# Kernel tuning notes

Measured on AMD Instinct MI355X. Metric: run time of the kernel, lower is better.

## Reference

```python
import jax, jax.numpy as jnp
import numpy as np

B, R, A, S, F, N = 2, 1, 16, 14, 1024, 512  # batch, num_rx, num_rx_ant, ofdm_symbols, fft_size, num_effective_sc
D = S * N  # flattened time-frequency dim that C acts on


def setup_inputs() -> dict:
    key = jax.random.key(0)
    k0, k1, k2, k3 = jax.random.split(key, 4)
    scale = 1.0 / np.sqrt(D).astype(np.float32)
    x_re = jax.random.normal(k0, (B, R, A, S, F), jnp.float32)
    x_im = jax.random.normal(k1, (B, R, A, S, F), jnp.float32)
    C_re = jax.random.normal(k2, (D, D), jnp.float32) * scale
    C_im = jax.random.normal(k3, (D, D), jnp.float32) * scale
    # unique, sorted effective-subcarrier indices (as in an OFDM ResourceGrid)
    sc_ind = jnp.asarray(np.sort(np.random.default_rng(0).choice(F, N, replace=False)), jnp.int32)
    return {"x_re": x_re, "x_im": x_im, "C_re": C_re, "C_im": C_im, "sc_ind": sc_ind}


def reference(x_re, x_im, C_re, C_im, sc_ind):
    x = jax.lax.complex(x_re, x_im)            # [B,R,A,S,F] complex64
    C = jax.lax.complex(C_re, C_im)            # [D,D]
    y = jnp.take(x, sc_ind, axis=-1)           # gather effective subcarriers -> [B,R,A,S,N]
    b, r, a, s, n = y.shape
    yf = y.reshape(b, r, a, s * n)             # flatten_last_dims(y, 2)
    # multiply_from_right with adjoint: yf @ C^H
    yf = jnp.einsum('brad,ed->brae', yf, jnp.conj(C))
    y = yf.reshape(b, r, a, s, n)
    # scatter back into full fft_size grid (unique indices -> set == scatter_nd on zeros)
    out = jnp.zeros((b, r, a, s, F), y.dtype).at[..., sc_ind].set(y)
    return jnp.stack([out.real, out.imag])     # [2,B,R,A,S,F] (real, imag)
```

## Files before the change

### kernel.cpp

```cpp
#include <hip/hip_runtime.h>
#include <hip/hip_bf16.h>

#define B_ 2
#define R_ 1
#define A_ 16
#define S_ 14
#define F_ 1024
#define N_ 512
#define D_ (S_*N_)
#define M_ (B_*R_*A_)
#define KK_ (2*D_)
#define BE 64
#define ETILES (D_/BE)

typedef __attribute__((ext_vector_type(8))) short bf16x8;
typedef __attribute__((ext_vector_type(4))) float f32x4;

static __device__ inline short f2bf(float f) {
    __hip_bfloat16 h = __float2bfloat16(f);
    return *reinterpret_cast<short*>(&h);
}
static __device__ inline float bf2f(short s) {
    unsigned int u = ((unsigned int)(unsigned short)s) << 16;
    return __uint_as_float(u);
}

#define LDSP(p) ((__attribute__((address_space(3))) void*)(p))
#define GLBP(p) ((const __attribute__((address_space(1))) void*)(p))

__global__ void prep_kernel(const float* __restrict__ xr, const float* __restrict__ xi,
                            const int* __restrict__ sc, short* __restrict__ Ap) {
    int idx = blockIdx.x * blockDim.x + threadIdx.x;
    if (idx >= 64 * KK_) return;
    int k = idx % KK_;
    int r = idx / KK_;
    int m = r & 31;
    int half = (k >= D_) ? 1 : 0;
    int d = half ? (k - D_) : k;
    int s = d >> 9;
    int n = d & 511;
    int f = sc[n];
    const float* base = (r < 32) ? (half ? xi : xr) : (half ? xr : xi);
    float v = base[(m * S_ + s) * F_ + f];
    if (r >= 32 && half) v = -v;
    Ap[((size_t)(k >> 3) * 64 + r) * 8 + (k & 7)] = f2bf(v);
}

__global__ void zero_kernel(float4* __restrict__ out, int n4) {
    int i = blockIdx.x * blockDim.x + threadIdx.x;
    if (i < n4) out[i] = make_float4(0.f, 0.f, 0.f, 0.f);
}

__global__ __launch_bounds__(256) void gemm_wasync(
    const short* __restrict__ Ap,
    const float* __restrict__ Cre, const float* __restrict__ Cim,
    short* __restrict__ part_all)
{
    constexpr int KSPLIT = 28;
    constexpr int KBLK = KK_ / KSPLIT;
    constexpr int NCH  = KBLK / 32;
    __shared__ float Bl[4][3][16 * 32];
    __shared__ short Al[4][3][64 * 32];

    const int etile = blockIdx.x;
    const int ks    = blockIdx.y;
    const int tid   = threadIdx.x;
    const int wave  = tid >> 6;
    const int lane  = tid & 63;
    const int l16   = lane & 15;
    const int kg    = lane >> 4;

    const float* Cp = (ks < 14) ? Cre : Cim;
    const int kc = (ks % 14) * KBLK;
    const int ka = ks * KBLK;

    const int U0 = lane, U1 = 64 + lane;
    const float* bsrc0 = Cp + (size_t)(etile * 64 + wave * 16 + (U0 >> 3)) * D_
                            + kc + ((U0 & 7) ^ ((U0 >> 3) & 7)) * 4;
    const float* bsrc1 = Cp + (size_t)(etile * 64 + wave * 16 + (U1 >> 3)) * D_
                            + kc + ((U1 & 7) ^ ((U1 >> 3) & 7)) * 4;
    const short* asrc = Ap + (size_t)(ka >> 3) * 512 + lane * 8;

#define WAITV(n) asm volatile("s_waitcnt vmcnt(" #n ")" ::: "memory")
#define STAGE(cc) do { \
        int bb = (cc) % 3; \
        __builtin_amdgcn_global_load_lds(GLBP(bsrc0 + (size_t)(cc) * 32), \
                                         LDSP(&Bl[wave][bb][lane * 4]), 16, 0, 0); \
        __builtin_amdgcn_global_load_lds(GLBP(bsrc1 + (size_t)(cc) * 32), \
                                         LDSP(&Bl[wave][bb][(64 + lane) * 4]), 16, 0, 0); \
        __builtin_amdgcn_global_load_lds(GLBP(asrc + (size_t)(cc) * 2048 + 0 * 512), \
                                         LDSP(&Al[wave][bb][lane * 8]), 16, 0, 0); \
        __builtin_amdgcn_global_load_lds(GLBP(asrc + (size_t)(cc) * 2048 + 1 * 512), \
                                         LDSP(&Al[wave][bb][(64 + lane) * 8]), 16, 0, 0); \
        __builtin_amdgcn_global_load_lds(GLBP(asrc + (size_t)(cc) * 2048 + 2 * 512), \
                                         LDSP(&Al[wave][bb][(128 + lane) * 8]), 16, 0, 0); \
        __builtin_amdgcn_global_load_lds(GLBP(asrc + (size_t)(cc) * 2048 + 3 * 512), \
                                         LDSP(&Al[wave][bb][(192 + lane) * 8]), 16, 0, 0); \
    } while (0)

    STAGE(0);
    STAGE(1);
    STAGE(2);

    f32x4 acc0 = {0.f,0.f,0.f,0.f}, acc1 = {0.f,0.f,0.f,0.f};
    f32x4 acc2 = {0.f,0.f,0.f,0.f}, acc3 = {0.f,0.f,0.f,0.f};

    const int swz  = l16 & 7;
    const int boff = l16 * 32;
    const int u0x = ((kg * 2 + 0) ^ swz) * 4;
    const int u1x = ((kg * 2 + 1) ^ swz) * 4;

    for (int c = 0; c < NCH; ++c) {
        if (c <= NCH - 3)      { WAITV(12); }
        else if (c == NCH - 2) { WAITV(6); }
        else                   { WAITV(0); }
        __builtin_amdgcn_sched_barrier(0);

        const int buf = c % 3;
        f32x4 b0 = *reinterpret_cast<const f32x4*>(&Bl[wave][buf][boff + u0x]);
        f32x4 b1 = *reinterpret_cast<const f32x4*>(&Bl[wave][buf][boff + u1x]);
        bf16x8 a0 = *reinterpret_cast<const bf16x8*>(&Al[wave][buf][(kg * 64 + 0 * 16 + l16) * 8]);
        bf16x8 a1 = *reinterpret_cast<const bf16x8*>(&Al[wave][buf][(kg * 64 + 1 * 16 + l16) * 8]);
        bf16x8 a2 = *reinterpret_cast<const bf16x8*>(&Al[wave][buf][(kg * 64 + 2 * 16 + l16) * 8]);
        bf16x8 a3 = *reinterpret_cast<const bf16x8*>(&Al[wave][buf][(kg * 64 + 3 * 16 + l16) * 8]);
        asm volatile("s_waitcnt lgkmcnt(0)" ::: "memory");
        __builtin_amdgcn_sched_barrier(0);

        if (c + 3 < NCH) STAGE(c + 3);
        __builtin_amdgcn_sched_barrier(0);

        bf16x8 bfv;
        bfv[0] = f2bf(b0.x); bfv[1] = f2bf(b0.y); bfv[2] = f2bf(b0.z); bfv[3] = f2bf(b0.w);
        bfv[4] = f2bf(b1.x); bfv[5] = f2bf(b1.y); bfv[6] = f2bf(b1.z); bfv[7] = f2bf(b1.w);
        acc0 = __builtin_amdgcn_mfma_f32_16x16x32_bf16(a0, bfv, acc0, 0, 0, 0);
        acc1 = __builtin_amdgcn_mfma_f32_16x16x32_bf16(a1, bfv, acc1, 0, 0, 0);
        acc2 = __builtin_amdgcn_mfma_f32_16x16x32_bf16(a2, bfv, acc2, 0, 0, 0);
        acc3 = __builtin_amdgcn_mfma_f32_16x16x32_bf16(a3, bfv, acc3, 0, 0, 0);
    }
#undef STAGE
#undef WAITV

    const int e_lane = etile * 64 + wave * 16 + l16;
    short* part = part_all + (size_t)ks * (64 * D_);
    #pragma unroll
    for (int mt = 0; mt < 4; ++mt) {
        f32x4 a = (mt == 0) ? acc0 : (mt == 1) ? acc1 : (mt == 2) ? acc2 : acc3;
        int rbase = mt * 16 + kg * 4;
        #pragma unroll
        for (int r = 0; r < 4; ++r)
            part[(size_t)(rbase + r) * D_ + e_lane] = f2bf(a[r]);
    }
}

template<int KSPLIT, int PARTIALS>
__global__ __launch_bounds__(256) void gemm_sync(
    const short* __restrict__ Ap,
    const float* __restrict__ Cre, const float* __restrict__ Cim,
    const int* __restrict__ sc,
    void* __restrict__ outp)
{
    constexpr int KBLK = KK_ / KSPLIT;
    constexpr int NCH  = KBLK / 32;
    __shared__ float Bls[3][64 * 32];
    __shared__ short Als[3][64 * 32];

    const int etile = blockIdx.x;
    const int ks    = blockIdx.y;
    const int tid   = threadIdx.x;
    const int wave  = tid >> 6;
    const int lane  = tid & 63;
    const int l16   = lane & 15;
    const int kg    = lane >> 4;

    const float* Cp = (ks < KSPLIT / 2) ? Cre : Cim;
    const int kc = (ks % (KSPLIT / 2)) * KBLK;
    const int ka = ks * KBLK;

    const float* bsrc[2];
    #pragma unroll
    for (int q = 0; q < 2; ++q) {
        int U = q * 256 + tid;
        int row = U >> 3;
        int u = (U & 7) ^ (row & 7);
        bsrc[q] = Cp + (size_t)(etile * BE + row) * D_ + kc + u * 4;
    }
    const short* asrc = Ap + ((size_t)(ka >> 3) * 64) * 8 + tid * 8;

#define STG(c) do { \
        int bf_ = (c) % 3; \
        __builtin_amdgcn_global_load_lds(GLBP(bsrc[0] + (size_t)(c) * 32), \
                                         LDSP(&Bls[bf_][(0 * 256 + tid) * 4]), 16, 0, 0); \
        __builtin_amdgcn_global_load_lds(GLBP(bsrc[1] + (size_t)(c) * 32), \
                                         LDSP(&Bls[bf_][(1 * 256 + tid) * 4]), 16, 0, 0); \
        __builtin_amdgcn_global_load_lds(GLBP(asrc + (size_t)(c) * 2048), \
                                         LDSP(&Als[bf_][tid * 8]), 16, 0, 0); \
    } while (0)

    STG(0);
    STG(1);

    f32x4 acc0 = {0.f,0.f,0.f,0.f}, acc1 = {0.f,0.f,0.f,0.f};
    f32x4 acc2 = {0.f,0.f,0.f,0.f}, acc3 = {0.f,0.f,0.f,0.f};

    const int row  = wave * 16 + l16;
    const int swz  = row & 7;
    const int boff = row * 32;
    const int u0 = ((kg * 2 + 0) ^ swz) * 4;
    const int u1 = ((kg * 2 + 1) ^ swz) * 4;

    for (int c = 0; c < NCH; ++c) {
        if (c < NCH - 1) asm volatile("s_waitcnt vmcnt(3)" ::: "memory");
        else             asm volatile("s_waitcnt vmcnt(0)" ::: "memory");
        __builtin_amdgcn_sched_barrier(0);
        __builtin_amdgcn_s_barrier();

        const int buf = c % 3;
        f32x4 b0 = *reinterpret_cast<const f32x4*>(&Bls[buf][boff + u0]);
        f32x4 b1 = *reinterpret_cast<const f32x4*>(&Bls[buf][boff + u1]);
        bf16x8 a0 = *reinterpret_cast<const bf16x8*>(&Als[buf][(kg * 64 + 0 * 16 + l16) * 8]);
        bf16x8 a1 = *reinterpret_cast<const bf16x8*>(&Als[buf][(kg * 64 + 1 * 16 + l16) * 8]);
        bf16x8 a2 = *reinterpret_cast<const bf16x8*>(&Als[buf][(kg * 64 + 2 * 16 + l16) * 8]);
        bf16x8 a3 = *reinterpret_cast<const bf16x8*>(&Als[buf][(kg * 64 + 3 * 16 + l16) * 8]);
        asm volatile("s_waitcnt lgkmcnt(0)" ::: "memory");
        __builtin_amdgcn_sched_barrier(0);
        __builtin_amdgcn_s_barrier();

        if (c + 2 < NCH) STG(c + 2);

        bf16x8 bfv;
        bfv[0] = f2bf(b0.x); bfv[1] = f2bf(b0.y); bfv[2] = f2bf(b0.z); bfv[3] = f2bf(b0.w);
        bfv[4] = f2bf(b1.x); bfv[5] = f2bf(b1.y); bfv[6] = f2bf(b1.z); bfv[7] = f2bf(b1.w);
        acc0 = __builtin_amdgcn_mfma_f32_16x16x32_bf16(a0, bfv, acc0, 0, 0, 0);
        acc1 = __builtin_amdgcn_mfma_f32_16x16x32_bf16(a1, bfv, acc1, 0, 0, 0);
        acc2 = __builtin_amdgcn_mfma_f32_16x16x32_bf16(a2, bfv, acc2, 0, 0, 0);
        acc3 = __builtin_amdgcn_mfma_f32_16x16x32_bf16(a3, bfv, acc3, 0, 0, 0);
    }
#undef STG

    const int e_lane = etile * BE + row;
    if (PARTIALS) {
        short* part = (short*)outp + (size_t)ks * (64 * D_);
        #pragma unroll
        for (int mt = 0; mt < 4; ++mt) {
            f32x4 a = (mt == 0) ? acc0 : (mt == 1) ? acc1 : (mt == 2) ? acc2 : acc3;
            int rbase = mt * 16 + kg * 4;
            #pragma unroll
            for (int r = 0; r < 4; ++r)
                part[(size_t)(rbase + r) * D_ + e_lane] = f2bf(a[r]);
        }
    } else {
        float* out = (float*)outp;
        int s = e_lane >> 9, n = e_lane & 511;
        int f = sc[n];
        #pragma unroll
        for (int mt = 0; mt < 4; ++mt) {
            f32x4 a = (mt == 0) ? acc0 : (mt == 1) ? acc1 : (mt == 2) ? acc2 : acc3;
            int rbase = mt * 16 + kg * 4;
            #pragma unroll
            for (int r = 0; r < 4; ++r) {
                int rr = rbase + r;
                int pp = rr >> 5, m = rr & 31;
                atomicAdd(&out[((pp * M_ + m) * S_ + s) * F_ + f], a[r]);
            }
        }
    }
}

template<int KSPLIT>
__global__ void reduce_kernel(const short* __restrict__ part, const int* __restrict__ sc,
                              float* __restrict__ out) {
    int t = blockIdx.x * blockDim.x + threadIdx.x;
    if (t >= 64 * D_ / 8) return;
    int base = t * 8;
    int e0 = base % D_;
    int r  = base / D_;
    float v[8] = {0.f,0.f,0.f,0.f,0.f,0.f,0.f,0.f};
    #pragma unroll
    for (int ksp = 0; ksp < KSPLIT; ++ksp) {
        bf16x8 x = *reinterpret_cast<const bf16x8*>(&part[(size_t)ksp * (64 * D_) + base]);
        #pragma unroll
        for (int j = 0; j < 8; ++j) v[j] += bf2f(x[j]);
    }
    int pp = r >> 5, m = r & 31, s = e0 >> 9, n0 = e0 & 511;
    float* ob = &out[((pp * M_ + m) * S_ + s) * F_];
    #pragma unroll
    for (int j = 0; j < 8; ++j) ob[sc[n0 + j]] = v[j];
}

extern "C" void kernel_launch(void* const* d_in, const int* in_sizes, int n_in,
                              void* d_out, int out_size, void* d_ws, size_t ws_size,
                              hipStream_t stream) {
    const float* xr  = (const float*)d_in[0];
    const float* xi  = (const float*)d_in[1];
    const float* Cre = (const float*)d_in[2];
    const float* Cim = (const float*)d_in[3];
    const int*   sc  = (const int*)d_in[4];
    float* out = (float*)d_out;

    short* Ap = (short*)d_ws;
    const size_t partOff = 2u * 1024u * 1024u;
    const size_t need28  = partOff + 28ull * 64 * D_ * 2;
    const size_t need16  = partOff + 16ull * 64 * D_ * 2;

    prep_kernel<<<dim3((64 * KK_ + 255) / 256), 256, 0, stream>>>(xr, xi, sc, Ap);
    zero_kernel<<<dim3((917504 / 4 + 255) / 256), 256, 0, stream>>>((float4*)out, 917504 / 4);

    const int rthreads = 64 * D_ / 8;
    if (ws_size >= need28) {
        short* part = (short*)((char*)d_ws + partOff);
        gemm_wasync<<<dim3(ETILES, 28), 256, 0, stream>>>(Ap, Cre, Cim, part);
        reduce_kernel<28><<<dim3((rthreads + 255) / 256), 256, 0, stream>>>(part, sc, out);
    } else if (ws_size >= need16) {
        short* part = (short*)((char*)d_ws + partOff);
        gemm_sync<16, 1><<<dim3(ETILES, 16), 256, 0, stream>>>(Ap, Cre, Cim, sc, part);
        reduce_kernel<16><<<dim3((rthreads + 255) / 256), 256, 0, stream>>>(part, sc, out);
    } else {
        gemm_sync<16, 0><<<dim3(ETILES, 16), 256, 0, stream>>>(Ap, Cre, Cim, sc, out);
    }
}
```

Baseline: 123.8 us.

## Load GEMM A operand directly into registers instead of staging through LDS

Result: faster. 118.9 us (-4.0%).

```diff
diff --git a/kernel.cpp b/kernel.cpp
--- a/kernel.cpp
+++ b/kernel.cpp
@@ -51,7 +51,7 @@
     if (i < n4) out[i] = make_float4(0.f, 0.f, 0.f, 0.f);
 }
 
-__global__ __launch_bounds__(256) void gemm_wasync(
+__global__ __launch_bounds__(256, 2) void gemm_areg(
     const short* __restrict__ Ap,
     const float* __restrict__ Cre, const float* __restrict__ Cim,
     short* __restrict__ part_all)
@@ -60,7 +60,6 @@
     constexpr int KBLK = KK_ / KSPLIT;
     constexpr int NCH  = KBLK / 32;
     __shared__ float Bl[4][3][16 * 32];
-    __shared__ short Al[4][3][64 * 32];
 
     const int etile = blockIdx.x;
     const int ks    = blockIdx.y;
@@ -79,7 +78,7 @@
                             + kc + ((U0 & 7) ^ ((U0 >> 3) & 7)) * 4;
     const float* bsrc1 = Cp + (size_t)(etile * 64 + wave * 16 + (U1 >> 3)) * D_
                             + kc + ((U1 & 7) ^ ((U1 >> 3) & 7)) * 4;
-    const short* asrc = Ap + (size_t)(ka >> 3) * 512 + lane * 8;
+    const short* abase = Ap + (((size_t)(ka >> 3) + kg) * 64 + l16) * 8;
 
 #define WAITV(n) asm volatile("s_waitcnt vmcnt(" #n ")" ::: "memory")
 #define STAGE(cc) do { \
@@ -88,19 +87,7 @@
                                          LDSP(&Bl[wave][bb][lane * 4]), 16, 0, 0); \
         __builtin_amdgcn_global_load_lds(GLBP(bsrc1 + (size_t)(cc) * 32), \
                                          LDSP(&Bl[wave][bb][(64 + lane) * 4]), 16, 0, 0); \
-        __builtin_amdgcn_global_load_lds(GLBP(asrc + (size_t)(cc) * 2048 + 0 * 512), \
-                                         LDSP(&Al[wave][bb][lane * 8]), 16, 0, 0); \
-        __builtin_amdgcn_global_load_lds(GLBP(asrc + (size_t)(cc) * 2048 + 1 * 512), \
-                                         LDSP(&Al[wave][bb][(64 + lane) * 8]), 16, 0, 0); \
-        __builtin_amdgcn_global_load_lds(GLBP(asrc + (size_t)(cc) * 2048 + 2 * 512), \
-                                         LDSP(&Al[wave][bb][(128 + lane) * 8]), 16, 0, 0); \
-        __builtin_amdgcn_global_load_lds(GLBP(asrc + (size_t)(cc) * 2048 + 3 * 512), \
-                                         LDSP(&Al[wave][bb][(192 + lane) * 8]), 16, 0, 0); \
     } while (0)
-
-    STAGE(0);
-    STAGE(1);
-    STAGE(2);
 
     f32x4 acc0 = {0.f,0.f,0.f,0.f}, acc1 = {0.f,0.f,0.f,0.f};
     f32x4 acc2 = {0.f,0.f,0.f,0.f}, acc3 = {0.f,0.f,0.f,0.f};
@@ -110,32 +97,68 @@
     const int u0x = ((kg * 2 + 0) ^ swz) * 4;
     const int u1x = ((kg * 2 + 1) ^ swz) * 4;
 
-    for (int c = 0; c < NCH; ++c) {
-        if (c <= NCH - 3)      { WAITV(12); }
-        else if (c == NCH - 2) { WAITV(6); }
-        else                   { WAITV(0); }
-        __builtin_amdgcn_sched_barrier(0);
-
+    bf16x8 areg[8][4];
+
+    #pragma unroll
+    for (int c8 = 0; c8 < 8; ++c8)
+        #pragma unroll
+        for (int mt = 0; mt < 4; ++mt)
+            areg[c8][mt] = *reinterpret_cast<const bf16x8*>(abase + (size_t)c8 * 2048 + mt * 128);
+    asm volatile("s_waitcnt vmcnt(0)" ::: "memory");
+    __builtin_amdgcn_sched_barrier(0);
+
+    STAGE(0);
+    STAGE(1);
+    STAGE(2);
+
+    #pragma unroll
+    for (int c = 0; c < 8; ++c) {
+        WAITV(4);
+        __builtin_amdgcn_sched_barrier(0);
         const int buf = c % 3;
         f32x4 b0 = *reinterpret_cast<const f32x4*>(&Bl[wave][buf][boff + u0x]);
         f32x4 b1 = *reinterpret_cast<const f32x4*>(&Bl[wave][buf][boff + u1x]);
-        bf16x8 a0 = *reinterpret_cast<const bf16x8*>(&Al[wave][buf][(kg * 64 + 0 * 16 + l16) * 8]);
-        bf16x8 a1 = *reinterpret_cast<const bf16x8*>(&Al[wave][buf][(kg * 64 + 1 * 16 + l16) * 8]);
-        bf16x8 a2 = *reinterpret_cast<const bf16x8*>(&Al[wave][buf][(kg * 64 + 2 * 16 + l16) * 8]);
-        bf16x8 a3 = *reinterpret_cast<const bf16x8*>(&Al[wave][buf][(kg * 64 + 3 * 16 + l16) * 8]);
         asm volatile("s_waitcnt lgkmcnt(0)" ::: "memory");
         __builtin_amdgcn_sched_barrier(0);
-
-        if (c + 3 < NCH) STAGE(c + 3);
-        __builtin_amdgcn_sched_barrier(0);
-
+        STAGE(c + 3);
+        __builtin_amdgcn_sched_barrier(0);
         bf16x8 bfv;
         bfv[0] = f2bf(b0.x); bfv[1] = f2bf(b0.y); bfv[2] = f2bf(b0.z); bfv[3] = f2bf(b0.w);
         bfv[4] = f2bf(b1.x); bfv[5] = f2bf(b1.y); bfv[6] = f2bf(b1.z); bfv[7] = f2bf(b1.w);
-        acc0 = __builtin_amdgcn_mfma_f32_16x16x32_bf16(a0, bfv, acc0, 0, 0, 0);
-        acc1 = __builtin_amdgcn_mfma_f32_16x16x32_bf16(a1, bfv, acc1, 0, 0, 0);
-        acc2 = __builtin_amdgcn_mfma_f32_16x16x32_bf16(a2, bfv, acc2, 0, 0, 0);
-        acc3 = __builtin_amdgcn_mfma_f32_16x16x32_bf16(a3, bfv, acc3, 0, 0, 0);
+        acc0 = __builtin_amdgcn_mfma_f32_16x16x32_bf16(areg[c][0], bfv, acc0, 0, 0, 0);
+        acc1 = __builtin_amdgcn_mfma_f32_16x16x32_bf16(areg[c][1], bfv, acc1, 0, 0, 0);
+        acc2 = __builtin_amdgcn_mfma_f32_16x16x32_bf16(areg[c][2], bfv, acc2, 0, 0, 0);
+        acc3 = __builtin_amdgcn_mfma_f32_16x16x32_bf16(areg[c][3], bfv, acc3, 0, 0, 0);
+    }
+
+    #pragma unroll
+    for (int c8 = 0; c8 < 8; ++c8)
+        #pragma unroll
+        for (int mt = 0; mt < 4; ++mt)
+            areg[c8][mt] = *reinterpret_cast<const bf16x8*>(abase + (size_t)(8 + c8) * 2048 + mt * 128);
+    asm volatile("s_waitcnt vmcnt(0)" ::: "memory");
+    __builtin_amdgcn_sched_barrier(0);
+
+    #pragma unroll
+    for (int c = 8; c < 16; ++c) {
+        if (c <= 13)      { WAITV(4); }
+        else if (c == 14) { WAITV(2); }
+        else              { WAITV(0); }
+        __builtin_amdgcn_sched_barrier(0);
+        const int buf = c % 3;
+        f32x4 b0 = *reinterpret_cast<const f32x4*>(&Bl[wave][buf][boff + u0x]);
+        f32x4 b1 = *reinterpret_cast<const f32x4*>(&Bl[wave][buf][boff + u1x]);
+        asm volatile("s_waitcnt lgkmcnt(0)" ::: "memory");
+        __builtin_amdgcn_sched_barrier(0);
+        if (c + 3 < NCH) STAGE(c + 3);
+        __builtin_amdgcn_sched_barrier(0);
+        bf16x8 bfv;
+        bfv[0] = f2bf(b0.x); bfv[1] = f2bf(b0.y); bfv[2] = f2bf(b0.z); bfv[3] = f2bf(b0.w);
+        bfv[4] = f2bf(b1.x); bfv[5] = f2bf(b1.y); bfv[6] = f2bf(b1.z); bfv[7] = f2bf(b1.w);
+        acc0 = __builtin_amdgcn_mfma_f32_16x16x32_bf16(areg[c - 8][0], bfv, acc0, 0, 0, 0);
+        acc1 = __builtin_amdgcn_mfma_f32_16x16x32_bf16(areg[c - 8][1], bfv, acc1, 0, 0, 0);
+        acc2 = __builtin_amdgcn_mfma_f32_16x16x32_bf16(areg[c - 8][2], bfv, acc2, 0, 0, 0);
+        acc3 = __builtin_amdgcn_mfma_f32_16x16x32_bf16(areg[c - 8][3], bfv, acc3, 0, 0, 0);
     }
 #undef STAGE
 #undef WAITV
@@ -308,7 +331,7 @@
     const int rthreads = 64 * D_ / 8;
     if (ws_size >= need28) {
         short* part = (short*)((char*)d_ws + partOff);
-        gemm_wasync<<<dim3(ETILES, 28), 256, 0, stream>>>(Ap, Cre, Cim, part);
+        gemm_areg<<<dim3(ETILES, 28), 256, 0, stream>>>(Ap, Cre, Cim, part);
         reduce_kernel<28><<<dim3((rthreads + 255) / 256), 256, 0, stream>>>(part, sc, out);
     } else if (ws_size >= need16) {
         short* part = (short*)((char*)d_ws + partOff);
```
